# Kernel tuning notes

Hardware: AMD Instinct MI355X
Metric: run time of the kernel (lower is better)

## Reference

```python
import jax, jax.numpy as jnp
import numpy as np

B, Q, K, F, H, D = 2, 4096, 4096, 512, 8, 64

def setup_inputs() -> dict:
    key = jax.random.key(0)
    ks = jax.random.split(key, 6)
    s = 1.0 / np.sqrt(F)
    return {
        "inputs_q": jax.random.normal(ks[0], (B, Q, F), dtype=jnp.float32),
        "inputs_kv": jax.random.normal(ks[1], (B, K, F), dtype=jnp.float32),
        "Wq": jax.random.normal(ks[2], (F, H, D), dtype=jnp.float32) * s,
        "Wk": jax.random.normal(ks[3], (F, H, D), dtype=jnp.float32) * s,
        "Wv": jax.random.normal(ks[4], (F, H, D), dtype=jnp.float32) * s,
        "Wo": jax.random.normal(ks[5], (H, D, F), dtype=jnp.float32) * (1.0 / np.sqrt(H * D)),
    }

def reference(inputs_q, inputs_kv, Wq, Wk, Wv, Wo):
    # QKV projections (DenseGeneral, no bias): [B, L, F] -> [B, L, H, D]
    q = jnp.einsum("bqf,fhd->bqhd", inputs_q, Wq)
    k = jnp.einsum("bkf,fhd->bkhd", inputs_kv, Wk)
    v = jnp.einsum("bkf,fhd->bkhd", inputs_kv, Wv)
    # Explicit attention matrix [B, H, Q, K] as in the original module
    logits = jnp.einsum("bqhd,bkhd->bhqk", q, k)
    attn = jax.nn.softmax(logits, axis=-1)
    out = jnp.einsum("bhqk,bkhd->bqhd", attn, v)
    # Output projection over (heads, head_dim): [B, Q, H, D] -> [B, Q, F]
    return jnp.einsum("bqhd,hdf->bqf", out, Wo)
```

## Files before the change

### kernel.cpp

```cpp
#include <hip/hip_runtime.h>
#include <hip/hip_bf16.h>

typedef short bf16x8 __attribute__((ext_vector_type(8)));
typedef _Float16 f16;
typedef f16 f16x8 __attribute__((ext_vector_type(8)));
typedef float f32x4 __attribute__((ext_vector_type(4)));
typedef unsigned short u16;
typedef u16 u16x8 __attribute__((ext_vector_type(8)));
typedef unsigned int u32;
typedef u32 u32x2 __attribute__((ext_vector_type(2)));

#define B_  2
#define L_  4096
#define F_  512
#define H_  8
#define D_  64
#define M_  8192
#define NSPL 2
#define KHALF (L_ / NSPL)

#define LOG2E 1.442695041f

__device__ inline u16 f2bf(float f) {
    union { float f; unsigned u; } v; v.f = f;
    unsigned r = v.u + 0x7fff + ((v.u >> 16) & 1);
    return (u16)(r >> 16);
}
__device__ inline u16 f2h(float f) {
    union { f16 h; u16 u; } v; v.h = (f16)f;
    return v.u;
}
__device__ inline float h2f(u16 u) {
    union { u16 u; f16 h; } v; v.u = u;
    return (float)v.h;
}

__global__ __launch_bounds__(256) void wt_kernel(
    const float* __restrict__ Wq, const float* __restrict__ Wk,
    const float* __restrict__ Wv, const float* __restrict__ Wo,
    u16* __restrict__ Tq, u16* __restrict__ Tk,
    u16* __restrict__ Tv, u16* __restrict__ To) {
    __shared__ float t[32][33];
    const int z = blockIdx.z;
    const float* in = (z == 0) ? Wq : (z == 1) ? Wk : (z == 2) ? Wv : Wo;
    u16* out = (z == 0) ? Tq : (z == 1) ? Tk : (z == 2) ? Tv : To;
    int k0 = blockIdx.y * 32, n0 = blockIdx.x * 32;
    int c = threadIdx.x & 31, r8 = threadIdx.x >> 5;
#pragma unroll
    for (int i = 0; i < 4; ++i) {
        int r = r8 * 4 + i;
        t[r][c] = in[(size_t)(k0 + r) * F_ + n0 + c];
    }
    __syncthreads();
#pragma unroll
    for (int i = 0; i < 4; ++i) {
        int r = r8 * 4 + i;
        out[(size_t)(n0 + r) * F_ + k0 + c] = f2h(t[c][r]);
    }
}

__global__ __launch_bounds__(256, 3) void proj_kernel(
    const float* __restrict__ Xq, const float* __restrict__ Xkv,
    const u16* __restrict__ Wqt, const u16* __restrict__ Wkt,
    const u16* __restrict__ Wvt,
    u16* __restrict__ Qw, u16* __restrict__ Kw, u16* __restrict__ Vw) {
    __shared__ u16 Ah[128][72];
    __shared__ u16 B1[64][72];
    __shared__ u16 B2[64][72];
    const int tid = threadIdx.x;
    const int w = tid >> 6, lane = tid & 63, lx = lane & 15, quad = lane >> 4;
    const int m0 = blockIdx.x * 128, n0 = blockIdx.y * 64;
    const bool isKV = (blockIdx.z == 1);
    const float* A = isKV ? Xkv : Xq;
    const u16* W1 = isKV ? Wkt : Wqt;

    float4 apre[8];
    u16x8 b1p[2], b2p[2];

    auto load_ab = [&](int k0) {
#pragma unroll
        for (int it = 0; it < 4; ++it) {
            int slot = tid + it * 256, r = slot >> 3, g = (slot & 7) * 8;
            apre[2 * it]     = *(const float4*)(A + (size_t)(m0 + r) * F_ + k0 + g);
            apre[2 * it + 1] = *(const float4*)(A + (size_t)(m0 + r) * F_ + k0 + g + 4);
        }
#pragma unroll
        for (int it = 0; it < 2; ++it) {
            int slot = tid + it * 256, r = slot >> 3, g = (slot & 7) * 8;
            b1p[it] = *(const u16x8*)(W1 + (size_t)(n0 + r) * F_ + k0 + g);
            if (isKV)
                b2p[it] = *(const u16x8*)(Wvt + (size_t)(n0 + r) * F_ + k0 + g);
        }
    };
    auto write_ab = [&]() {
#pragma unroll
        for (int it = 0; it < 4; ++it) {
            int slot = tid + it * 256, r = slot >> 3, g = (slot & 7) * 8;
            float4 f0 = apre[2 * it], f1 = apre[2 * it + 1];
            u16 th[8] = {f2h(f0.x), f2h(f0.y), f2h(f0.z), f2h(f0.w),
                         f2h(f1.x), f2h(f1.y), f2h(f1.z), f2h(f1.w)};
            *(u16x8*)&Ah[r][g] = *(u16x8*)th;
        }
#pragma unroll
        for (int it = 0; it < 2; ++it) {
            int slot = tid + it * 256, r = slot >> 3, g = (slot & 7) * 8;
            *(u16x8*)&B1[r][g] = b1p[it];
            if (isKV) *(u16x8*)&B2[r][g] = b2p[it];
        }
    };

    f32x4 acc1[2][4] = {}, acc2[2][4] = {};

    load_ab(0);
    write_ab();
    __syncthreads();
    load_ab(64);

    for (int k0 = 0; k0 < F_; k0 += 64) {
#pragma unroll
        for (int ks = 0; ks < 2; ++ks) {
            f16x8 af[2];
#pragma unroll
            for (int mf = 0; mf < 2; ++mf)
                af[mf] = *(const f16x8*)&Ah[w * 32 + mf * 16 + lx][ks * 32 + quad * 8];
#pragma unroll
            for (int nt = 0; nt < 4; ++nt) {
                f16x8 b1 = *(const f16x8*)&B1[nt * 16 + lx][ks * 32 + quad * 8];
#pragma unroll
                for (int mf = 0; mf < 2; ++mf)
                    acc1[mf][nt] = __builtin_amdgcn_mfma_f32_16x16x32_f16(af[mf], b1, acc1[mf][nt], 0, 0, 0);
                if (isKV) {
                    f16x8 b2 = *(const f16x8*)&B2[nt * 16 + lx][ks * 32 + quad * 8];
#pragma unroll
                    for (int mf = 0; mf < 2; ++mf)
                        acc2[mf][nt] = __builtin_amdgcn_mfma_f32_16x16x32_f16(af[mf], b2, acc2[mf][nt], 0, 0, 0);
                }
            }
        }
        if (k0 < F_ - 64) {
            __syncthreads();
            write_ab();
            __syncthreads();
            if (k0 < F_ - 128) load_ab(k0 + 128);
        }
    }

    const int h = n0 >> 6;
    const float scl = isKV ? 1.0f : LOG2E;
    u16* C1 = isKV ? Kw : Qw;
#pragma unroll
    for (int mf = 0; mf < 2; ++mf)
#pragma unroll
        for (int nt = 0; nt < 4; ++nt)
#pragma unroll
            for (int i = 0; i < 4; ++i) {
                int m = m0 + w * 32 + mf * 16 + quad * 4 + i;
                int b = m >> 12, l = m & 4095;
                int d = nt * 16 + lx;
                C1[((size_t)(b * H_ + h) * L_ + l) * D_ + d] = f2h(acc1[mf][nt][i] * scl);
            }
    if (isKV) {
        __syncthreads();
#pragma unroll
        for (int mf = 0; mf < 2; ++mf)
#pragma unroll
            for (int nt = 0; nt < 4; ++nt)
#pragma unroll
                for (int i = 0; i < 4; ++i)
                    Ah[w * 32 + mf * 16 + quad * 4 + i][nt * 16 + lx] = f2bf(acc2[mf][nt][i]);
        __syncthreads();
        int d = tid >> 2, seg = (tid & 3) * 32;
        int b = m0 >> 12;
        u16 tmp[32];
#pragma unroll
        for (int j = 0; j < 32; ++j) tmp[j] = Ah[seg + j][d];
        size_t base = ((size_t)(b * H_ + h) * D_ + d) * L_ + (m0 & 4095) + seg;
#pragma unroll
        for (int c = 0; c < 4; ++c)
            *(u16x8*)(Vw + base + c * 8) = *(u16x8*)&tmp[c * 8];
    }
}

__global__ __launch_bounds__(256) void out_gemm(const u16* __restrict__ A16,
                                                const u16* __restrict__ Wt,
                                                float* __restrict__ Cf) {
    __shared__ u16 As[128][72];
    __shared__ u16 Bs[128][72];
    const int tid = threadIdx.x;
    const int w = tid >> 6, lane = tid & 63, lx = lane & 15, quad = lane >> 4;
    const int m0 = blockIdx.x * 128, n0 = blockIdx.y * 128;

    u16x8 a16p[4];
    u16x8 bp[4];

    auto load_ab = [&](int k0) {
#pragma unroll
        for (int it = 0; it < 4; ++it) {
            int slot = tid + it * 256, r = slot >> 3, g = (slot & 7) * 8;
            a16p[it] = *(const u16x8*)(A16 + (size_t)(m0 + r) * F_ + k0 + g);
            bp[it]   = *(const u16x8*)(Wt  + (size_t)(n0 + r) * F_ + k0 + g);
        }
    };
    auto write_ab = [&]() {
#pragma unroll
        for (int it = 0; it < 4; ++it) {
            int slot = tid + it * 256, r = slot >> 3, g = (slot & 7) * 8;
            *(u16x8*)&As[r][g] = a16p[it];
            *(u16x8*)&Bs[r][g] = bp[it];
        }
    };

    f32x4 acc[2][8] = {};

    load_ab(0);
    write_ab();
    __syncthreads();
    load_ab(64);

    for (int k0 = 0; k0 < F_; k0 += 64) {
#pragma unroll
        for (int ks = 0; ks < 2; ++ks) {
            f16x8 af[2];
#pragma unroll
            for (int mf = 0; mf < 2; ++mf)
                af[mf] = *(const f16x8*)&As[w * 32 + mf * 16 + lx][ks * 32 + quad * 8];
#pragma unroll
            for (int nt = 0; nt < 8; ++nt) {
                f16x8 bf = *(const f16x8*)&Bs[nt * 16 + lx][ks * 32 + quad * 8];
#pragma unroll
                for (int mf = 0; mf < 2; ++mf)
                    acc[mf][nt] = __builtin_amdgcn_mfma_f32_16x16x32_f16(af[mf], bf, acc[mf][nt], 0, 0, 0);
            }
        }
        if (k0 < F_ - 64) {
            __syncthreads();
            write_ab();
            __syncthreads();
            if (k0 < F_ - 128) load_ab(k0 + 128);
        }
    }

#pragma unroll
    for (int mf = 0; mf < 2; ++mf)
#pragma unroll
        for (int nt = 0; nt < 8; ++nt)
#pragma unroll
            for (int i = 0; i < 4; ++i) {
                int m = m0 + w * 32 + mf * 16 + quad * 4 + i;
                int n = n0 + nt * 16 + lx;
                Cf[(size_t)m * F_ + n] = acc[mf][nt][i];
            }
}

__global__ __launch_bounds__(256, 2) void flash_mfma(
    const u16* __restrict__ Qg, const u16* __restrict__ Kg,
    const u16* __restrict__ Vtg, u16* __restrict__ On, float* __restrict__ Ls) {
    __shared__ u16 Ks[2][64][72];
    __shared__ u16 Vs[2][64][72];

    const int tid = threadIdx.x;
    const int w = tid >> 6, lane = tid & 63, lx = lane & 15, quad = lane >> 4;

    const int x = blockIdx.x;
    const int t = x >> 3;
    const int hh = t >> 5;
    const int s = (t >> 4) & 1;
    const int bh = (x & 7) * 2 + hh;
    const int q0 = (t & 15) * 256;

    const u16* Qp = Qg + ((size_t)bh * L_ + q0) * D_;
    const u16* Kp = Kg + (size_t)bh * L_ * D_ + (size_t)(s * KHALF) * D_;
    const u16* Vp = Vtg + (size_t)bh * D_ * L_ + s * KHALF;

    f16x8 qreg[4][2];
#pragma unroll
    for (int qf = 0; qf < 4; ++qf)
#pragma unroll
        for (int ks = 0; ks < 2; ++ks)
            qreg[qf][ks] = *(const f16x8*)(Qp + (size_t)(w * 64 + qf * 16 + lx) * D_ +
                                           ks * 32 + quad * 8);

    u16x8 kp[2], vp[2];
    auto load_kv = [&](int kt) {
#pragma unroll
        for (int it = 0; it < 2; ++it) {
            int slot = tid + it * 256, r = slot >> 3, g = (slot & 7) * 8;
            kp[it] = *(const u16x8*)(Kp + (size_t)(kt * 64 + r) * D_ + g);
            vp[it] = *(const u16x8*)(Vp + (size_t)r * L_ + kt * 64 + g);
        }
    };
    auto write_kv = [&](int p) {
#pragma unroll
        for (int it = 0; it < 2; ++it) {
            int slot = tid + it * 256, r = slot >> 3, g = (slot & 7) * 8;
            *(u16x8*)&Ks[p][r][g] = kp[it];
            *(u16x8*)&Vs[p][r][g] = vp[it];
        }
    };

    const bf16x8 vone = {0x3F80, 0x3F80, 0x3F80, 0x3F80,
                         0x3F80, 0x3F80, 0x3F80, 0x3F80};
    f32x4 o[4][4] = {};
    f32x4 osum[4] = {};

    load_kv(0);
    write_kv(0);
    __syncthreads();
    load_kv(1);

    const int NT = KHALF / 64;
    for (int kt = 0; kt < NT; ++kt) {
        const int p = kt & 1;

        f32x4 sv[4][4] = {};
#pragma unroll
        for (int ks = 0; ks < 2; ++ks)
#pragma unroll
            for (int nt = 0; nt < 4; ++nt) {
                f16x8 ak = *(const f16x8*)&Ks[p][nt * 16 + lx][ks * 32 + quad * 8];
#pragma unroll
                for (int qf = 0; qf < 4; ++qf)
                    sv[nt][qf] = __builtin_amdgcn_mfma_f32_16x16x32_f16(ak, qreg[qf][ks], sv[nt][qf], 0, 0, 0);
            }

        if (kt < NT - 1) write_kv(p ^ 1);

        bf16x8 ap0[4], ap1[4];
#pragma unroll
        for (int half = 0; half < 2; ++half)
#pragma unroll
            for (int qf = 0; qf < 4; ++qf) {
                u32 pu[2], pw[2];
#pragma unroll
                for (int n = 0; n < 2; ++n) {
                    u32 ub[4];
#pragma unroll
                    for (int i = 0; i < 4; ++i)
                        ub[i] = __float_as_uint(__builtin_amdgcn_exp2f(sv[half * 2 + n][qf][i]));
                    pu[n] = __builtin_amdgcn_perm(ub[1], ub[0], 0x07060302u);
                    pw[n] = __builtin_amdgcn_perm(ub[3], ub[2], 0x07060302u);
                }
                u32x2 r  = __builtin_amdgcn_permlane32_swap(pu[0], pu[1], false, false);
                u32x2 r2 = __builtin_amdgcn_permlane16_swap(r[0], r[1], false, false);
                u32x2 tt = __builtin_amdgcn_permlane32_swap(pw[0], pw[1], false, false);
                u32x2 t2 = __builtin_amdgcn_permlane16_swap(tt[0], tt[1], false, false);
                union { u32 d[4]; bf16x8 h; } cvt;
                cvt.d[0] = r2[0];
                cvt.d[1] = t2[0];
                cvt.d[2] = r2[1];
                cvt.d[3] = t2[1];
                if (half == 0) ap0[qf] = cvt.h; else ap1[qf] = cvt.h;
            }

        __builtin_amdgcn_s_setprio(1);
#pragma unroll
        for (int qf = 0; qf < 4; ++qf)
            osum[qf] = __builtin_amdgcn_mfma_f32_16x16x32_bf16(ap0[qf], vone, osum[qf], 0, 0, 0);
#pragma unroll
        for (int nt = 0; nt < 4; ++nt) {
            bf16x8 bv = *(const bf16x8*)&Vs[p][nt * 16 + lx][quad * 8];
#pragma unroll
            for (int qf = 0; qf < 4; ++qf)
                o[qf][nt] = __builtin_amdgcn_mfma_f32_16x16x32_bf16(ap0[qf], bv, o[qf][nt], 0, 0, 0);
        }
#pragma unroll
        for (int qf = 0; qf < 4; ++qf)
            osum[qf] = __builtin_amdgcn_mfma_f32_16x16x32_bf16(ap1[qf], vone, osum[qf], 0, 0, 0);
#pragma unroll
        for (int nt = 0; nt < 4; ++nt) {
            bf16x8 bv = *(const bf16x8*)&Vs[p][nt * 16 + lx][32 + quad * 8];
#pragma unroll
            for (int qf = 0; qf < 4; ++qf)
                o[qf][nt] = __builtin_amdgcn_mfma_f32_16x16x32_bf16(ap1[qf], bv, o[qf][nt], 0, 0, 0);
        }
        __builtin_amdgcn_s_setprio(0);

        if (kt < NT - 1) __syncthreads();
        if (kt < NT - 2) load_kv(kt + 2);
    }

    const int b = bh >> 3, h = bh & 7;
    u16* Op = On + (size_t)s * M_ * F_;
#pragma unroll
    for (int qf = 0; qf < 4; ++qf) {
        float linv[4];
#pragma unroll
        for (int i = 0; i < 4; ++i) linv[i] = 1.f / osum[qf][i];
#pragma unroll
        for (int nt = 0; nt < 4; ++nt)
#pragma unroll
            for (int i = 0; i < 4; ++i) {
                int l = q0 + w * 64 + qf * 16 + quad * 4 + i;
                Op[((size_t)b * L_ + l) * (H_ * D_) + h * D_ + nt * 16 + lx] =
                    f2h(o[qf][nt][i] * linv[i]);
            }
        if (lx == 0) {
            float* lp = Ls + ((size_t)s * (B_ * H_) + bh) * L_ +
                        q0 + w * 64 + qf * 16 + quad * 4;
#pragma unroll
            for (int i = 0; i < 4; ++i) lp[i] = osum[qf][i];
        }
    }
}

__global__ __launch_bounds__(256) void reduce_kernel(
    const u16* __restrict__ On, const float* __restrict__ Ls,
    u16* __restrict__ Ow) {
    int gid = blockIdx.x * 256 + threadIdx.x;
    size_t off = (size_t)gid * 8;
    int row = gid >> 3;
    int b = row >> 15, rem = row & 32767;
    int l = rem >> 3, h = rem & 7;
    int lidx = ((b * H_ + h) << 12) + l;
    float l1 = Ls[lidx], l2 = Ls[B_ * H_ * L_ + lidx];
    float w1 = l1 / (l1 + l2), w2 = 1.f - w1;
    u16x8 a = *(const u16x8*)(On + off);
    u16x8 c = *(const u16x8*)(On + (size_t)M_ * F_ + off);
    u16 r[8];
#pragma unroll
    for (int j = 0; j < 8; ++j)
        r[j] = f2h(w1 * h2f(a[j]) + w2 * h2f(c[j]));
    *(u16x8*)(Ow + off) = *(u16x8*)r;
}

extern "C" void kernel_launch(void* const* d_in, const int* in_sizes, int n_in,
                              void* d_out, int out_size, void* d_ws, size_t ws_size,
                              hipStream_t stream)
{
    const float* Xq  = (const float*)d_in[0];
    const float* Xkv = (const float*)d_in[1];
    const float* Wq  = (const float*)d_in[2];
    const float* Wk  = (const float*)d_in[3];
    const float* Wv  = (const float*)d_in[4];
    const float* Wo  = (const float*)d_in[5];
    float* out = (float*)d_out;

    u16* ws  = (u16*)d_ws;
    const size_t MF = (size_t)M_ * F_;
    const size_t FF = (size_t)F_ * F_;
    u16* Wqt = ws;
    u16* Wkt = Wqt + FF;
    u16* Wvt = Wkt + FF;
    u16* Wot = Wvt + FF;
    u16* Qw  = Wot + FF;
    u16* Kw  = Qw + MF;
    u16* Vw  = Kw + MF;
    u16* On  = Vw + MF;
    float* Ls = (float*)(On + 2 * MF);
    u16* Ow  = Qw;

    wt_kernel<<<dim3(16, 16, 4), 256, 0, stream>>>(Wq, Wk, Wv, Wo,
                                                   Wqt, Wkt, Wvt, Wot);

    proj_kernel<<<dim3(64, 8, 2), 256, 0, stream>>>(Xq, Xkv, Wqt, Wkt, Wvt,
                                                    Qw, Kw, Vw);

    flash_mfma<<<dim3(512), 256, 0, stream>>>(Qw, Kw, Vw, On, Ls);

    reduce_kernel<<<dim3((int)(MF / 8 / 256)), 256, 0, stream>>>(On, Ls, Ow);

    out_gemm<<<dim3(64, 4), 256, 0, stream>>>(Ow, Wot, out);
}
```

Baseline: 200.4 us.

## Split K/V projection into separate blocks and interleave softmax with MFMA in attention

The projection kernel now launches a third z-slice so K and V are computed by separate blocks rather than one block doing both. This drops the second LDS B tile and accumulator set, giving more balanced blocks and lower register and LDS pressure at the cost of reloading Xkv. In the flash kernel, the exp2/permute softmax conversion for the first half of the key tile now runs interleaved with the QK MFMAs of the second half, and the second half's conversion is interleaved with the PV MFMAs of the first half. The aim is to overlap VALU and transcendental work with matrix-core work, with V fragments hoisted into registers, at some cost in register pressure.

```diff
diff --git a/kernel.cpp b/kernel.cpp
--- a/kernel.cpp
+++ b/kernel.cpp
@@ -66,16 +66,15 @@
     u16* __restrict__ Qw, u16* __restrict__ Kw, u16* __restrict__ Vw) {
     __shared__ u16 Ah[128][72];
     __shared__ u16 B1[64][72];
-    __shared__ u16 B2[64][72];
     const int tid = threadIdx.x;
     const int w = tid >> 6, lane = tid & 63, lx = lane & 15, quad = lane >> 4;
     const int m0 = blockIdx.x * 128, n0 = blockIdx.y * 64;
-    const bool isKV = (blockIdx.z == 1);
-    const float* A = isKV ? Xkv : Xq;
-    const u16* W1 = isKV ? Wkt : Wqt;
+    const int z = blockIdx.z;
+    const float* A = (z == 0) ? Xq : Xkv;
+    const u16* W1 = (z == 0) ? Wqt : (z == 1) ? Wkt : Wvt;
 
     float4 apre[8];
-    u16x8 b1p[2], b2p[2];
+    u16x8 b1p[2];
 
     auto load_ab = [&](int k0) {
 #pragma unroll
@@ -88,8 +87,6 @@
         for (int it = 0; it < 2; ++it) {
             int slot = tid + it * 256, r = slot >> 3, g = (slot & 7) * 8;
             b1p[it] = *(const u16x8*)(W1 + (size_t)(n0 + r) * F_ + k0 + g);
-            if (isKV)
-                b2p[it] = *(const u16x8*)(Wvt + (size_t)(n0 + r) * F_ + k0 + g);
         }
     };
     auto write_ab = [&]() {
@@ -105,11 +102,10 @@
         for (int it = 0; it < 2; ++it) {
             int slot = tid + it * 256, r = slot >> 3, g = (slot & 7) * 8;
             *(u16x8*)&B1[r][g] = b1p[it];
-            if (isKV) *(u16x8*)&B2[r][g] = b2p[it];
-        }
-    };
-
-    f32x4 acc1[2][4] = {}, acc2[2][4] = {};
+        }
+    };
+
+    f32x4 acc1[2][4] = {};
 
     load_ab(0);
     write_ab();
@@ -129,12 +125,6 @@
 #pragma unroll
                 for (int mf = 0; mf < 2; ++mf)
                     acc1[mf][nt] = __builtin_amdgcn_mfma_f32_16x16x32_f16(af[mf], b1, acc1[mf][nt], 0, 0, 0);
-                if (isKV) {
-                    f16x8 b2 = *(const f16x8*)&B2[nt * 16 + lx][ks * 32 + quad * 8];
-#pragma unroll
-                    for (int mf = 0; mf < 2; ++mf)
-                        acc2[mf][nt] = __builtin_amdgcn_mfma_f32_16x16x32_f16(af[mf], b2, acc2[mf][nt], 0, 0, 0);
-                }
             }
         }
         if (k0 < F_ - 64) {
@@ -146,20 +136,21 @@
     }
 
     const int h = n0 >> 6;
-    const float scl = isKV ? 1.0f : LOG2E;
-    u16* C1 = isKV ? Kw : Qw;
-#pragma unroll
-    for (int mf = 0; mf < 2; ++mf)
-#pragma unroll
-        for (int nt = 0; nt < 4; ++nt)
-#pragma unroll
-            for (int i = 0; i < 4; ++i) {
-                int m = m0 + w * 32 + mf * 16 + quad * 4 + i;
-                int b = m >> 12, l = m & 4095;
-                int d = nt * 16 + lx;
-                C1[((size_t)(b * H_ + h) * L_ + l) * D_ + d] = f2h(acc1[mf][nt][i] * scl);
-            }
-    if (isKV) {
+    if (z < 2) {
+        const float scl = (z == 0) ? LOG2E : 1.0f;
+        u16* C1 = (z == 0) ? Qw : Kw;
+#pragma unroll
+        for (int mf = 0; mf < 2; ++mf)
+#pragma unroll
+            for (int nt = 0; nt < 4; ++nt)
+#pragma unroll
+                for (int i = 0; i < 4; ++i) {
+                    int m = m0 + w * 32 + mf * 16 + quad * 4 + i;
+                    int b = m >> 12, l = m & 4095;
+                    int d = nt * 16 + lx;
+                    C1[((size_t)(b * H_ + h) * L_ + l) * D_ + d] = f2h(acc1[mf][nt][i] * scl);
+                }
+    } else {
         __syncthreads();
 #pragma unroll
         for (int mf = 0; mf < 2; ++mf)
@@ -167,7 +158,7 @@
             for (int nt = 0; nt < 4; ++nt)
 #pragma unroll
                 for (int i = 0; i < 4; ++i)
-                    Ah[w * 32 + mf * 16 + quad * 4 + i][nt * 16 + lx] = f2bf(acc2[mf][nt][i]);
+                    Ah[w * 32 + mf * 16 + quad * 4 + i][nt * 16 + lx] = f2bf(acc1[mf][nt][i]);
         __syncthreads();
         int d = tid >> 2, seg = (tid & 3) * 32;
         int b = m0 >> 12;
@@ -298,6 +289,29 @@
         }
     };
 
+    auto smqf = [&](const f32x4& s0, const f32x4& s1) -> bf16x8 {
+        u32 ub0[4], ub1[4];
+#pragma unroll
+        for (int i = 0; i < 4; ++i) {
+            ub0[i] = __float_as_uint(__builtin_amdgcn_exp2f(s0[i]));
+            ub1[i] = __float_as_uint(__builtin_amdgcn_exp2f(s1[i]));
+        }
+        u32 pu0 = __builtin_amdgcn_perm(ub0[1], ub0[0], 0x07060302u);
+        u32 pw0 = __builtin_amdgcn_perm(ub0[3], ub0[2], 0x07060302u);
+        u32 pu1 = __builtin_amdgcn_perm(ub1[1], ub1[0], 0x07060302u);
+        u32 pw1 = __builtin_amdgcn_perm(ub1[3], ub1[2], 0x07060302u);
+        u32x2 r  = __builtin_amdgcn_permlane32_swap(pu0, pu1, false, false);
+        u32x2 r2 = __builtin_amdgcn_permlane16_swap(r[0], r[1], false, false);
+        u32x2 tt = __builtin_amdgcn_permlane32_swap(pw0, pw1, false, false);
+        u32x2 t2 = __builtin_amdgcn_permlane16_swap(tt[0], tt[1], false, false);
+        union { u32 d[4]; bf16x8 h; } cvt;
+        cvt.d[0] = r2[0];
+        cvt.d[1] = t2[0];
+        cvt.d[2] = r2[1];
+        cvt.d[3] = t2[1];
+        return cvt.h;
+    };
+
     const bf16x8 vone = {0x3F80, 0x3F80, 0x3F80, 0x3F80,
                          0x3F80, 0x3F80, 0x3F80, 0x3F80};
     f32x4 o[4][4] = {};
@@ -316,62 +330,60 @@
 #pragma unroll
         for (int ks = 0; ks < 2; ++ks)
 #pragma unroll
-            for (int nt = 0; nt < 4; ++nt) {
+            for (int nt = 0; nt < 2; ++nt) {
                 f16x8 ak = *(const f16x8*)&Ks[p][nt * 16 + lx][ks * 32 + quad * 8];
 #pragma unroll
                 for (int qf = 0; qf < 4; ++qf)
                     sv[nt][qf] = __builtin_amdgcn_mfma_f32_16x16x32_f16(ak, qreg[qf][ks], sv[nt][qf], 0, 0, 0);
             }
 
+        f16x8 akB[2][2];
+#pragma unroll
+        for (int ks = 0; ks < 2; ++ks)
+#pragma unroll
+            for (int nt = 0; nt < 2; ++nt)
+                akB[ks][nt] = *(const f16x8*)&Ks[p][(nt + 2) * 16 + lx][ks * 32 + quad * 8];
+
+        bf16x8 apA[4];
+#pragma unroll
+        for (int qf = 0; qf < 4; ++qf) {
+            sv[2][qf] = __builtin_amdgcn_mfma_f32_16x16x32_f16(akB[0][0], qreg[qf][0], sv[2][qf], 0, 0, 0);
+            sv[3][qf] = __builtin_amdgcn_mfma_f32_16x16x32_f16(akB[0][1], qreg[qf][0], sv[3][qf], 0, 0, 0);
+            sv[2][qf] = __builtin_amdgcn_mfma_f32_16x16x32_f16(akB[1][0], qreg[qf][1], sv[2][qf], 0, 0, 0);
+            sv[3][qf] = __builtin_amdgcn_mfma_f32_16x16x32_f16(akB[1][1], qreg[qf][1], sv[3][qf], 0, 0, 0);
+            apA[qf] = smqf(sv[0][qf], sv[1][qf]);
+        }
+
         if (kt < NT - 1) write_kv(p ^ 1);
 
-        bf16x8 ap0[4], ap1[4];
-#pragma unroll
-        for (int half = 0; half < 2; ++half)
-#pragma unroll
-            for (int qf = 0; qf < 4; ++qf) {
-                u32 pu[2], pw[2];
-#pragma unroll
-                for (int n = 0; n < 2; ++n) {
-                    u32 ub[4];
-#pragma unroll
-                    for (int i = 0; i < 4; ++i)
-                        ub[i] = __float_as_uint(__builtin_amdgcn_exp2f(sv[half * 2 + n][qf][i]));
-                    pu[n] = __builtin_amdgcn_perm(ub[1], ub[0], 0x07060302u);
-                    pw[n] = __builtin_amdgcn_perm(ub[3], ub[2], 0x07060302u);
-                }
-                u32x2 r  = __builtin_amdgcn_permlane32_swap(pu[0], pu[1], false, false);
-                u32x2 r2 = __builtin_amdgcn_permlane16_swap(r[0], r[1], false, false);
-                u32x2 tt = __builtin_amdgcn_permlane32_swap(pw[0], pw[1], false, false);
-                u32x2 t2 = __builtin_amdgcn_permlane16_swap(tt[0], tt[1], false, false);
-                union { u32 d[4]; bf16x8 h; } cvt;
-                cvt.d[0] = r2[0];
-                cvt.d[1] = t2[0];
-                cvt.d[2] = r2[1];
-                cvt.d[3] = t2[1];
-                if (half == 0) ap0[qf] = cvt.h; else ap1[qf] = cvt.h;
-            }
+        bf16x8 bvA[4];
+#pragma unroll
+        for (int nt = 0; nt < 4; ++nt)
+            bvA[nt] = *(const bf16x8*)&Vs[p][nt * 16 + lx][quad * 8];
 
         __builtin_amdgcn_s_setprio(1);
+        bf16x8 apB[4];
+#pragma unroll
+        for (int qf = 0; qf < 4; ++qf) {
+            osum[qf] = __builtin_amdgcn_mfma_f32_16x16x32_bf16(apA[qf], vone, osum[qf], 0, 0, 0);
+#pragma unroll
+            for (int nt = 0; nt < 4; ++nt)
+                o[qf][nt] = __builtin_amdgcn_mfma_f32_16x16x32_bf16(apA[qf], bvA[nt], o[qf][nt], 0, 0, 0);
+            apB[qf] = smqf(sv[2][qf], sv[3][qf]);
+        }
+
+        bf16x8 bvB[4];
+#pragma unroll
+        for (int nt = 0; nt < 4; ++nt)
+            bvB[nt] = *(const bf16x8*)&Vs[p][nt * 16 + lx][32 + quad * 8];
 #pragma unroll
         for (int qf = 0; qf < 4; ++qf)
-            osum[qf] = __builtin_amdgcn_mfma_f32_16x16x32_bf16(ap0[qf], vone, osum[qf], 0, 0, 0);
+            osum[qf] = __builtin_amdgcn_mfma_f32_16x16x32_bf16(apB[qf], vone, osum[qf], 0, 0, 0);
 #pragma unroll
         for (int nt = 0; nt < 4; ++nt) {
-            bf16x8 bv = *(const bf16x8*)&Vs[p][nt * 16 + lx][quad * 8];
 #pragma unroll
             for (int qf = 0; qf < 4; ++qf)
-                o[qf][nt] = __builtin_amdgcn_mfma_f32_16x16x32_bf16(ap0[qf], bv, o[qf][nt], 0, 0, 0);
-        }
-#pragma unroll
-        for (int qf = 0; qf < 4; ++qf)
-            osum[qf] = __builtin_amdgcn_mfma_f32_16x16x32_bf16(ap1[qf], vone, osum[qf], 0, 0, 0);
-#pragma unroll
-        for (int nt = 0; nt < 4; ++nt) {
-            bf16x8 bv = *(const bf16x8*)&Vs[p][nt * 16 + lx][32 + quad * 8];
-#pragma unroll
-            for (int qf = 0; qf < 4; ++qf)
-                o[qf][nt] = __builtin_amdgcn_mfma_f32_16x16x32_bf16(ap1[qf], bv, o[qf][nt], 0, 0, 0);
+                o[qf][nt] = __builtin_amdgcn_mfma_f32_16x16x32_bf16(apB[qf], bvB[nt], o[qf][nt], 0, 0, 0);
         }
         __builtin_amdgcn_s_setprio(0);
 
@@ -452,7 +464,7 @@
     wt_kernel<<<dim3(16, 16, 4), 256, 0, stream>>>(Wq, Wk, Wv, Wo,
                                                    Wqt, Wkt, Wvt, Wot);
 
-    proj_kernel<<<dim3(64, 8, 2), 256, 0, stream>>>(Xq, Xkv, Wqt, Wkt, Wvt,
+    proj_kernel<<<dim3(64, 8, 3), 256, 0, stream>>>(Xq, Xkv, Wqt, Wkt, Wvt,
                                                     Qw, Kw, Vw);
 
     flash_mfma<<<dim3(512), 256, 0, stream>>>(Qw, Kw, Vw, On, Ls);
```

After: 198.4 us. Within noise of the previous version (-1.0%).
